# Optimization experiments

Measured on AMD Instinct MI355X. Metric: run time of the kernel, lower is better.

The kernel has to match this reference:

```python
import jax, jax.numpy as jnp
import numpy as np

B, S, H, OUT = 64, 513, 1024, 128   # batch, seq (incl CLS), hidden, slot labels
T = S - 1                            # subword tokens after dropping [CLS]
P_WORD_START = 0.75                  # avg ~1.33 subwords per word


def setup_inputs() -> dict:
    key = jax.random.key(0)
    k1, k2, k3, k4 = jax.random.split(key, 4)
    hidden_states = jax.random.normal(k1, (B, S, H), jnp.float32)
    W = jax.random.normal(k2, (H, OUT), jnp.float32) * 0.02
    b = jax.random.normal(k3, (OUT,), jnp.float32) * 0.02
    # contiguous, non-decreasing word ids: cumsum of word-start flags
    starts = (jax.random.uniform(k4, (B, T)) < P_WORD_START).astype(jnp.int32)
    starts = starts.at[:, 0].set(1)
    segment_ids = jnp.cumsum(starts, axis=-1) - 1  # [B, T], values in [0, n_words)
    return {"hidden_states": hidden_states, "W": W, "b": b,
            "segment_ids": segment_ids}


def _merge_row(logits, seg):
    # logits: [T, OUT], seg: [T] contiguous non-decreasing word ids
    s = jax.ops.segment_sum(logits, seg, num_segments=T)                    # [T, OUT]
    c = jax.ops.segment_sum(jnp.ones((T,), logits.dtype), seg, num_segments=T)
    mean = s / jnp.maximum(c, 1.0)[:, None]
    # words beyond n_words (empty segments) -> zero padding, as in the original
    return jnp.where(c[:, None] > 0, mean, 0.0)


def reference(hidden_states, W, b, segment_ids):
    x = hidden_states[:, 1:]                       # drop [CLS]; dropout = identity (eval)
    logits = jnp.einsum('bth,ho->bto', x, W) + b   # [B, T, OUT]
    merged = jax.vmap(_merge_row)(logits, segment_ids)  # per-word ragged mean + pad
    return jnp.transpose(merged, (0, 2, 1))        # [B, OUT, T]
```

## Files before the change

kernel.cpp:

```cpp
#include <hip/hip_runtime.h>
#include <hip/hip_bf16.h>

#define B_    64
#define S_    513
#define T_    512
#define H_    1024
#define OUT_  128

#define BM 64
#define BN 128
#define BK 32
#define NKT (H_ / BK)

typedef __attribute__((ext_vector_type(8))) short short8_t;
typedef __attribute__((ext_vector_type(4))) float f32x4;

__device__ inline ushort f2bf(float f) {
    union { float f; unsigned u; } x; x.f = f;
    unsigned r = x.u + 0x7fffu + ((x.u >> 16) & 1u);
    return (ushort)(r >> 16);
}
__device__ inline float bf2f(ushort u) {
    union { unsigned u; float f; } x; x.u = (unsigned)u << 16; return x.f;
}

__global__ __launch_bounds__(256) void wt_kernel(
    const float* __restrict__ W, ushort* __restrict__ Wt)
{
    __shared__ ushort tile[64][65];
    int k0 = blockIdx.x * 64, o0 = blockIdx.y * 64;
    int tid = threadIdx.x;
#pragma unroll
    for (int p = 0; p < 16; ++p) {
        int idx = tid + p * 256;
        int r = idx >> 6, c = idx & 63;
        tile[r][c] = f2bf(W[(size_t)(k0 + r) * OUT_ + o0 + c]);
    }
    __syncthreads();
#pragma unroll
    for (int p = 0; p < 16; ++p) {
        int idx = tid + p * 256;
        int c = idx >> 6, r = idx & 63;
        Wt[(size_t)(o0 + c) * H_ + k0 + r] = tile[r][c];
    }
}

__global__ __launch_bounds__(256) void gemm_kernel(
    const float* __restrict__ hs, const ushort* __restrict__ Wt,
    ushort* __restrict__ logits)
{
    __shared__ __align__(16) ushort As[2][BM * BK];
    __shared__ __align__(16) ushort Bs[2][BN * BK];

    int blk = blockIdx.x;
    int b   = blk >> 3;
    int t0  = (blk & 7) * BM;
    int tid = threadIdx.x;
    int lane = tid & 63;
    int wv = tid >> 6;
    int wm = wv & 1, wn = wv >> 1;
    int l15 = lane & 15, ksl = lane >> 4;

    int rowA = tid >> 2;
    int cblk = tid & 3;
    int rowB1 = rowA + 64;

    const float*  aptr  = hs + ((size_t)(b * S_ + 1 + t0) + rowA) * H_ + cblk * 8;
    const ushort* bptr0 = Wt + (size_t)rowA  * H_ + cblk * 8;
    const ushort* bptr1 = Wt + (size_t)rowB1 * H_ + cblk * 8;

    auto swz = [](int row, int blkc) {
        return row * BK + ((blkc ^ ((row >> 1) & 3)) << 3);
    };
    int wAo  = swz(rowA, cblk);
    int wB0o = swz(rowA, cblk);
    int wB1o = swz(rowB1, cblk);

    int rAo[2], rBo[4];
#pragma unroll
    for (int fm = 0; fm < 2; ++fm) {
        int row = wm * 32 + fm * 16 + l15;
        rAo[fm] = swz(row, ksl);
    }
#pragma unroll
    for (int fn = 0; fn < 4; ++fn) {
        int row = wn * 64 + fn * 16 + l15;
        rBo[fn] = swz(row, ksl);
    }

    f32x4 acc[2][4];
#pragma unroll
    for (int fm = 0; fm < 2; ++fm)
#pragma unroll
        for (int fn = 0; fn < 4; ++fn) acc[fm][fn] = (f32x4){0.f, 0.f, 0.f, 0.f};

    float4 ra0, ra1;
    int4 rb0, rb1;

    auto loadT = [&](int kt) {
        const float* ap = aptr + kt * BK;
        ra0 = *reinterpret_cast<const float4*>(ap);
        ra1 = *reinterpret_cast<const float4*>(ap + 4);
        rb0 = *reinterpret_cast<const int4*>(bptr0 + kt * BK);
        rb1 = *reinterpret_cast<const int4*>(bptr1 + kt * BK);
    };
    auto writeT = [&](int nb) {
        union { ushort u[8]; int4 i; } pa;
        pa.u[0] = f2bf(ra0.x); pa.u[1] = f2bf(ra0.y);
        pa.u[2] = f2bf(ra0.z); pa.u[3] = f2bf(ra0.w);
        pa.u[4] = f2bf(ra1.x); pa.u[5] = f2bf(ra1.y);
        pa.u[6] = f2bf(ra1.z); pa.u[7] = f2bf(ra1.w);
        *reinterpret_cast<int4*>(&As[nb][wAo])  = pa.i;
        *reinterpret_cast<int4*>(&Bs[nb][wB0o]) = rb0;
        *reinterpret_cast<int4*>(&Bs[nb][wB1o]) = rb1;
    };
    auto computeT = [&](int cb) {
        short8_t af[2], bf[4];
#pragma unroll
        for (int fm = 0; fm < 2; ++fm)
            af[fm] = *reinterpret_cast<const short8_t*>(&As[cb][rAo[fm]]);
#pragma unroll
        for (int fn = 0; fn < 4; ++fn)
            bf[fn] = *reinterpret_cast<const short8_t*>(&Bs[cb][rBo[fn]]);
#pragma unroll
        for (int fm = 0; fm < 2; ++fm)
#pragma unroll
            for (int fn = 0; fn < 4; ++fn)
                acc[fm][fn] = __builtin_amdgcn_mfma_f32_16x16x32_bf16(
                    af[fm], bf[fn], acc[fm][fn], 0, 0, 0);
    };

    loadT(0);
    writeT(0);
    __syncthreads();

    for (int kt = 0; kt < NKT; ++kt) {
        int cb = kt & 1;
        if (kt + 1 < NKT) loadT(kt + 1);
        computeT(cb);
        if (kt + 1 < NKT) writeT(cb ^ 1);
        __syncthreads();
    }

#pragma unroll
    for (int fn = 0; fn < 4; ++fn) {
        int o = wn * 64 + fn * 16 + l15;
#pragma unroll
        for (int fm = 0; fm < 2; ++fm) {
#pragma unroll
            for (int r = 0; r < 4; ++r) {
                int t = t0 + wm * 32 + fm * 16 + ksl * 4 + r;
                logits[((size_t)b * T_ + t) * OUT_ + o] = f2bf(acc[fm][fn][r]);
            }
        }
    }
}

__global__ __launch_bounds__(256) void merge_kernel(
    const ushort* __restrict__ logits, const int* __restrict__ seg,
    const float* __restrict__ bias, float* __restrict__ out)
{
    int blk = blockIdx.x;
    int b   = blk >> 3;
    int s0  = (blk & 7) * 64;
    int tid = threadIdx.x;

    __shared__ int   sstart[64];
    __shared__ int   scnt[64];
    __shared__ float tile[OUT_][65];

    if (tid < 64) { sstart[tid] = T_; scnt[tid] = 0; }
    __syncthreads();
#pragma unroll
    for (int p = 0; p < 2; ++p) {
        int t = tid + p * 256;
        int li = seg[b * T_ + t] - s0;
        if (li >= 0 && li < 64) {
            atomicMin(&sstart[li], t);
            atomicAdd(&scnt[li], 1);
        }
    }
    __syncthreads();

#pragma unroll
    for (int it = 0; it < 32; ++it) {
        int idx = tid + it * 256;
        int sl  = idx >> 7;
        int o   = idx & 127;
        int c   = scnt[sl];
        float v = 0.f;
        if (c > 0) {
            int st = sstart[sl];
            const ushort* src = logits + ((size_t)b * T_ + st) * OUT_ + o;
            float sum = 0.f;
            for (int i = 0; i < c; ++i) sum += bf2f(src[(size_t)i * OUT_]);
            v = sum / (float)c + bias[o];
        }
        tile[o][sl] = v;
    }
    __syncthreads();

#pragma unroll
    for (int p = 0; p < 32; ++p) {
        int o  = (tid >> 6) + p * 4;
        int sl = tid & 63;
        out[((size_t)b * OUT_ + o) * T_ + s0 + sl] = tile[o][sl];
    }
}

extern "C" void kernel_launch(void* const* d_in, const int* in_sizes, int n_in,
                              void* d_out, int out_size, void* d_ws, size_t ws_size,
                              hipStream_t stream) {
    const float* hs   = (const float*)d_in[0];
    const float* W    = (const float*)d_in[1];
    const float* bias = (const float*)d_in[2];
    const int*   seg  = (const int*)d_in[3];
    float* out = (float*)d_out;

    ushort* logits = (ushort*)d_ws;
    ushort* Wt     = logits + (size_t)B_ * T_ * OUT_;

    wt_kernel<<<dim3(H_ / 64, OUT_ / 64), 256, 0, stream>>>(W, Wt);
    gemm_kernel<<<B_ * (T_ / BM), 256, 0, stream>>>(hs, Wt, logits);
    merge_kernel<<<B_ * (T_ / 64), 256, 0, stream>>>(logits, seg, bias, out);
}
```

Baseline: 57.33 us.

## Halve GEMM row tile, deepen register prefetch, use packed bf16 convert

The GEMM row tile is cut from 64 to 32 rows, which doubles the number of blocks. Each of the four waves now owns a 32-column slice of the outputs, and the launch bounds ask for four blocks per CU. Shared memory moves from an XOR swizzle to a padded k-chunk-major layout, global loads are prefetched two tiles ahead in registers, and fp32 to bf16 conversion uses the hardware v_cvt_pk_bf16_f32 instruction instead of software rounding. The goal is more in-flight memory traffic and better latency hiding on this bandwidth-bound projection. In exchange, each block reuses the W tile over fewer rows and needs more prefetch registers.

```diff
diff --git a/kernel.cpp b/kernel.cpp
--- a/kernel.cpp
+++ b/kernel.cpp
@@ -7,10 +7,13 @@
 #define H_    1024
 #define OUT_  128
 
-#define BM 64
+#define BM 32
 #define BN 128
 #define BK 32
 #define NKT (H_ / BK)
+
+#define ACS 272
+#define BCS 1040
 
 typedef __attribute__((ext_vector_type(8))) short short8_t;
 typedef __attribute__((ext_vector_type(4))) float f32x4;
@@ -22,6 +25,12 @@
 }
 __device__ inline float bf2f(ushort u) {
     union { unsigned u; float f; } x; x.u = (unsigned)u << 16; return x.f;
+}
+__device__ inline uint2 cvt4(const float4& v) {
+    uint2 r;
+    asm("v_cvt_pk_bf16_f32 %0, %1, %2" : "=v"(r.x) : "v"(v.x), "v"(v.y));
+    asm("v_cvt_pk_bf16_f32 %0, %1, %2" : "=v"(r.y) : "v"(v.z), "v"(v.w));
+    return r;
 }
 
 __global__ __launch_bounds__(256) void wt_kernel(
@@ -45,111 +54,95 @@
     }
 }
 
-__global__ __launch_bounds__(256) void gemm_kernel(
+__global__ __launch_bounds__(256, 4) void gemm_kernel(
     const float* __restrict__ hs, const ushort* __restrict__ Wt,
     ushort* __restrict__ logits)
 {
-    __shared__ __align__(16) ushort As[2][BM * BK];
-    __shared__ __align__(16) ushort Bs[2][BN * BK];
+    __shared__ __align__(16) ushort As[2][4 * ACS];
+    __shared__ __align__(16) ushort Bs[2][4 * BCS];
 
     int blk = blockIdx.x;
-    int b   = blk >> 3;
-    int t0  = (blk & 7) * BM;
+    int b   = blk >> 4;
+    int t0  = (blk & 15) * BM;
     int tid = threadIdx.x;
     int lane = tid & 63;
-    int wv = tid >> 6;
-    int wm = wv & 1, wn = wv >> 1;
-    int l15 = lane & 15, ksl = lane >> 4;
-
-    int rowA = tid >> 2;
-    int cblk = tid & 3;
-    int rowB1 = rowA + 64;
-
-    const float*  aptr  = hs + ((size_t)(b * S_ + 1 + t0) + rowA) * H_ + cblk * 8;
-    const ushort* bptr0 = Wt + (size_t)rowA  * H_ + cblk * 8;
-    const ushort* bptr1 = Wt + (size_t)rowB1 * H_ + cblk * 8;
-
-    auto swz = [](int row, int blkc) {
-        return row * BK + ((blkc ^ ((row >> 1) & 3)) << 3);
+    int w    = tid >> 6;
+    int l15  = lane & 15, ksl = lane >> 4;
+
+    int arow = tid >> 3, ac2 = tid & 7;
+    const float* aptr = hs + ((size_t)(b * S_ + 1 + t0 + arow)) * H_ + ac2 * 4;
+    int wAo = (ac2 >> 1) * ACS + arow * 8 + (ac2 & 1) * 4;
+
+    int brow = tid >> 1, bc = (tid & 1) * 2;
+    const ushort* bptr = Wt + (size_t)brow * H_ + bc * 8;
+    int wBo0 = bc * BCS + brow * 8;
+    int wBo1 = wBo0 + BCS;
+
+    int rAo[2], rBo[2];
+#pragma unroll
+    for (int fm = 0; fm < 2; ++fm) rAo[fm] = ksl * ACS + (fm * 16 + l15) * 8;
+#pragma unroll
+    for (int fn = 0; fn < 2; ++fn)
+        rBo[fn] = ksl * BCS + (w * 32 + fn * 16 + l15) * 8;
+
+    f32x4 acc[2][2];
+#pragma unroll
+    for (int fm = 0; fm < 2; ++fm)
+#pragma unroll
+        for (int fn = 0; fn < 2; ++fn) acc[fm][fn] = (f32x4){0.f, 0.f, 0.f, 0.f};
+
+    float4 ra[2];
+    int4   rb0[2], rb1[2];
+
+    auto LD = [&](int s, int kt) {
+        const float* ap = aptr + kt * BK;
+        ra[s]  = *reinterpret_cast<const float4*>(ap);
+        const ushort* bp = bptr + kt * BK;
+        rb0[s] = *reinterpret_cast<const int4*>(bp);
+        rb1[s] = *reinterpret_cast<const int4*>(bp + 8);
     };
-    int wAo  = swz(rowA, cblk);
-    int wB0o = swz(rowA, cblk);
-    int wB1o = swz(rowB1, cblk);
-
-    int rAo[2], rBo[4];
-#pragma unroll
-    for (int fm = 0; fm < 2; ++fm) {
-        int row = wm * 32 + fm * 16 + l15;
-        rAo[fm] = swz(row, ksl);
-    }
-#pragma unroll
-    for (int fn = 0; fn < 4; ++fn) {
-        int row = wn * 64 + fn * 16 + l15;
-        rBo[fn] = swz(row, ksl);
-    }
-
-    f32x4 acc[2][4];
-#pragma unroll
-    for (int fm = 0; fm < 2; ++fm)
-#pragma unroll
-        for (int fn = 0; fn < 4; ++fn) acc[fm][fn] = (f32x4){0.f, 0.f, 0.f, 0.f};
-
-    float4 ra0, ra1;
-    int4 rb0, rb1;
-
-    auto loadT = [&](int kt) {
-        const float* ap = aptr + kt * BK;
-        ra0 = *reinterpret_cast<const float4*>(ap);
-        ra1 = *reinterpret_cast<const float4*>(ap + 4);
-        rb0 = *reinterpret_cast<const int4*>(bptr0 + kt * BK);
-        rb1 = *reinterpret_cast<const int4*>(bptr1 + kt * BK);
+    auto WR = [&](int nb, int s) {
+        *reinterpret_cast<uint2*>(&As[nb][wAo]) = cvt4(ra[s]);
+        *reinterpret_cast<int4*>(&Bs[nb][wBo0]) = rb0[s];
+        *reinterpret_cast<int4*>(&Bs[nb][wBo1]) = rb1[s];
     };
-    auto writeT = [&](int nb) {
-        union { ushort u[8]; int4 i; } pa;
-        pa.u[0] = f2bf(ra0.x); pa.u[1] = f2bf(ra0.y);
-        pa.u[2] = f2bf(ra0.z); pa.u[3] = f2bf(ra0.w);
-        pa.u[4] = f2bf(ra1.x); pa.u[5] = f2bf(ra1.y);
-        pa.u[6] = f2bf(ra1.z); pa.u[7] = f2bf(ra1.w);
-        *reinterpret_cast<int4*>(&As[nb][wAo])  = pa.i;
-        *reinterpret_cast<int4*>(&Bs[nb][wB0o]) = rb0;
-        *reinterpret_cast<int4*>(&Bs[nb][wB1o]) = rb1;
-    };
-    auto computeT = [&](int cb) {
-        short8_t af[2], bf[4];
+    auto COMPUTE = [&](int cb) {
+        short8_t af[2], bf[2];
 #pragma unroll
         for (int fm = 0; fm < 2; ++fm)
             af[fm] = *reinterpret_cast<const short8_t*>(&As[cb][rAo[fm]]);
 #pragma unroll
-        for (int fn = 0; fn < 4; ++fn)
+        for (int fn = 0; fn < 2; ++fn)
             bf[fn] = *reinterpret_cast<const short8_t*>(&Bs[cb][rBo[fn]]);
 #pragma unroll
         for (int fm = 0; fm < 2; ++fm)
 #pragma unroll
-            for (int fn = 0; fn < 4; ++fn)
+            for (int fn = 0; fn < 2; ++fn)
                 acc[fm][fn] = __builtin_amdgcn_mfma_f32_16x16x32_bf16(
                     af[fm], bf[fn], acc[fm][fn], 0, 0, 0);
     };
 
-    loadT(0);
-    writeT(0);
-    __syncthreads();
+    LD(0, 0); LD(1, 1);
+    WR(0, 0);
+    __syncthreads();
+    LD(0, 2);
 
     for (int kt = 0; kt < NKT; ++kt) {
-        int cb = kt & 1;
-        if (kt + 1 < NKT) loadT(kt + 1);
-        computeT(cb);
-        if (kt + 1 < NKT) writeT(cb ^ 1);
+        COMPUTE(kt & 1);
+        int s = (kt + 1) & 1;
+        if (kt + 1 < NKT) WR(s, s);
+        if (kt + 3 < NKT) LD(s, kt + 3);
         __syncthreads();
     }
 
 #pragma unroll
-    for (int fn = 0; fn < 4; ++fn) {
-        int o = wn * 64 + fn * 16 + l15;
+    for (int fn = 0; fn < 2; ++fn) {
+        int o = w * 32 + fn * 16 + l15;
 #pragma unroll
         for (int fm = 0; fm < 2; ++fm) {
 #pragma unroll
             for (int r = 0; r < 4; ++r) {
-                int t = t0 + wm * 32 + fm * 16 + ksl * 4 + r;
+                int t = t0 + fm * 16 + ksl * 4 + r;
                 logits[((size_t)b * T_ + t) * OUT_ + o] = f2bf(acc[fm][fn][r]);
             }
         }
```

After: 113.4 us. +97.9%, slower.
